# Performance work log

Hardware: AMD Instinct MI355X
Metric: run time of the kernel (lower is better)

The kernel has to match this reference:

```python
import jax, jax.numpy as jnp
import numpy as np

B, C, H, W = 8, 512, 64, 64
HEADS = 8
R = 4  # reduction_ratio: depthwise conv kernel=stride=R, padding=R//2
EPS = 1e-5


def _conv(x, w, stride=1, pad=0, groups=1):
    # NCHW / OIHW conv
    return jax.lax.conv_general_dilated(
        x, w, (stride, stride), ((pad, pad), (pad, pad)),
        feature_group_count=groups)


def _layernorm_ch(x, g, b):
    # channel-wise LayerNorm over dim=1 (biased variance, as torch.var(unbiased=False))
    mean = jnp.mean(x, axis=1, keepdims=True)
    var = jnp.var(x, axis=1, keepdims=True)
    return (x - mean) / jnp.sqrt(var + EPS) * g + b


def _to_kv(t, wkv_dw, ln_g, ln_b, wkv_pw):
    t = _conv(t, wkv_dw, stride=R, pad=R // 2, groups=C)  # depthwise strided conv
    t = _layernorm_ch(t, ln_g, ln_b)
    return _conv(t, wkv_pw)  # 1x1 pointwise


def _split_heads(t):
    # 'b (h c) x y -> (b h) (x y) c'
    b, c, x, y = t.shape
    d = c // HEADS
    return t.reshape(b, HEADS, d, x * y).transpose(0, 1, 3, 2).reshape(b * HEADS, x * y, d)


def setup_inputs() -> dict:
    key = jax.random.key(0)
    ks = jax.random.split(key, 7)
    sem = jax.random.normal(ks[0], (B, C, H, W), jnp.float32)
    spa = jax.random.normal(ks[1], (B, C, H, W), jnp.float32)
    x = jax.random.normal(ks[2], (B, C, H, W), jnp.float32)
    wq = jax.random.normal(ks[3], (C, C, 1, 1), jnp.float32) * 0.02
    wkv_dw = jax.random.normal(ks[4], (C, 1, R, R), jnp.float32) * 0.02  # depthwise, groups=C
    ln_g = jnp.ones((1, C, 1, 1), jnp.float32)
    ln_b = jnp.zeros((1, C, 1, 1), jnp.float32)
    wkv_pw = jax.random.normal(ks[5], (C, C, 1, 1), jnp.float32) * 0.02
    wout = jax.random.normal(ks[6], (C, C, 1, 1), jnp.float32) * 0.02
    return {"sem": sem, "spa": spa, "x": x, "wq": wq, "wkv_dw": wkv_dw,
            "ln_g": ln_g, "ln_b": ln_b, "wkv_pw": wkv_pw, "wout": wout}


def reference(sem, spa, x, wq, wkv_dw, ln_g, ln_b, wkv_pw, wout):
    h, w = x.shape[-2:]
    scale = (C // HEADS) ** -0.5
    q = _conv(sem, wq)                               # [B,C,H,W]
    k = _to_kv(spa, wkv_dw, ln_g, ln_b, wkv_pw)      # [B,C,H',W'] downsampled
    v = _to_kv(x, wkv_dw, ln_g, ln_b, wkv_pw)
    q, k, v = map(_split_heads, (q, k, v))           # [(B*h), N, d]
    dots = jnp.einsum('bid,bjd->bij', q, k) * scale  # [(B*h), Nq, Nk]
    attn = jax.nn.softmax(dots, axis=-1)
    out = jnp.einsum('bij,bjd->bid', attn, v)        # [(B*h), Nq, d]
    # '(b h) (x y) c -> b (h c) x y'
    d = C // HEADS
    out = out.reshape(B, HEADS, h * w, d).transpose(0, 1, 3, 2).reshape(B, C, h, w)
    return _conv(out, wout)
```

## Files before the change

kernel.cpp:

```cpp
#include <hip/hip_runtime.h>
#include <hip/hip_bf16.h>


#define BATCH 8
#define CH 512
#define HW 4096
#define NHEADS 8
#define HD 64
#define PP 289
#define NKP 320

typedef __attribute__((ext_vector_type(8))) short bf16x8;
typedef __attribute__((ext_vector_type(4))) float f32x4;

__device__ inline float sanitize(float x) {
    unsigned u = __float_as_uint(x);
    if ((u & 0x7F800000u) == 0x7F800000u) return 0.0f;
    return x;
}
__device__ inline float ldin(const void* p, size_t i, int f32) {
    float x = f32 ? ((const float*)p)[i]
                  : __bfloat162float(((const __hip_bfloat16*)p)[i]);
    return sanitize(x);
}
__device__ inline void stout(void* p, size_t i, float v, int f32) {
    if (f32) ((float*)p)[i] = v;
    else     ((__hip_bfloat16*)p)[i] = __float2bfloat16(v);
}
__device__ inline short f2bf(float x) {
    unsigned u = __float_as_uint(x);
    unsigned r = (u + 0x7FFFu + ((u >> 16) & 1u)) >> 16;
    return (short)r;
}
__device__ inline float bf2f(short s) {
    unsigned u = ((unsigned)(unsigned short)s) << 16;
    return __uint_as_float(u);
}
__device__ inline void gload_lds16(const void* g, void* l) {
    __builtin_amdgcn_global_load_lds(
        (const __attribute__((address_space(1))) void*)g,
        (__attribute__((address_space(3))) void*)l, 16, 0, 0);
}

__global__ void detect_dtype(const unsigned short* __restrict__ w, int* __restrict__ flag) {
    __shared__ int red[256];
    int tid = threadIdx.x;
    int cnt = 0;
    for (int i = tid; i < 8192; i += 256) {
        unsigned e = w[i] & 0x7F80u;
        cnt += (e >= 0x4300u) ? 1 : 0;
    }
    red[tid] = cnt;
    __syncthreads();
    for (int o = 128; o; o >>= 1) { if (tid < o) red[tid] += red[tid + o]; __syncthreads(); }
    if (tid == 0) *flag = (red[0] > 500) ? 1 : 0;
}

__global__ __launch_bounds__(256)
void cvt_w(const void* __restrict__ in, short* __restrict__ out, const int* __restrict__ flag) {
    const int f32 = *flag;
    int i = (blockIdx.x * 256 + threadIdx.x) * 8;
#pragma unroll
    for (int e = 0; e < 8; ++e) out[i + e] = f2bf(ldin(in, i + e, f32));
}

__global__ __launch_bounds__(256)
void wprep(const void* __restrict__ w, const void* __restrict__ g, const void* __restrict__ bb,
           short* __restrict__ wg, float* __restrict__ ws, float* __restrict__ wb,
           const int* __restrict__ flag) {
    const int f32 = *flag;
    const int tid = threadIdx.x;
    const int wave = tid >> 6, lane = tid & 63;
    const int m = blockIdx.x * 4 + wave;
    float s = 0.f, sb = 0.f;
    union { alignas(16) short sh[8]; int4 v; } u;
#pragma unroll
    for (int e = 0; e < 8; ++e) {
        int c = lane * 8 + e;
        float wv = ldin(w, (size_t)m * CH + c, f32);
        float gv = ldin(g, c, f32);
        float bv = ldin(bb, c, f32);
        float p = wv * gv;
        u.sh[e] = f2bf(p);
        s += p;
        sb += wv * bv;
    }
    *(int4*)(wg + (size_t)m * CH + lane * 8) = u.v;
#pragma unroll
    for (int o = 1; o < 64; o <<= 1) {
        s += __shfl_xor(s, o, 64);
        sb += __shfl_xor(sb, o, 64);
    }
    if (lane == 0) { ws[m] = s; wb[m] = sb; }
}

__global__ __launch_bounds__(256)
void transpose_cvt(const void* __restrict__ in, short* __restrict__ outT,
                   const int* __restrict__ flag) {
    __shared__ short T[64 * 72];
    const int f32 = *flag;
    const int tid = threadIdx.x;
    const int z = blockIdx.z;
    const int c0 = blockIdx.y * 64, p0 = blockIdx.x * 64;
    {
        int c = tid >> 2, ps = (tid & 3) * 16;
        size_t src = ((size_t)z * CH + c0 + c) * HW + p0 + ps;
        short* dst = &T[c * 72 + ps];
        if (f32) {
            const float4* fp = (const float4*)((const float*)in + src);
#pragma unroll
            for (int v = 0; v < 4; ++v) {
                float4 w4 = fp[v];
                dst[v * 4 + 0] = f2bf(sanitize(w4.x));
                dst[v * 4 + 1] = f2bf(sanitize(w4.y));
                dst[v * 4 + 2] = f2bf(sanitize(w4.z));
                dst[v * 4 + 3] = f2bf(sanitize(w4.w));
            }
        } else {
            const int4* ip = (const int4*)((const short*)in + src);
#pragma unroll
            for (int v = 0; v < 2; ++v) {
                union { int4 q; short s[8]; } u; u.q = ip[v];
#pragma unroll
                for (int e = 0; e < 8; ++e) {
                    short sv = u.s[e];
                    if ((sv & 0x7F80) == 0x7F80) sv = 0;
                    dst[v * 8 + e] = sv;
                }
            }
        }
    }
    __syncthreads();
    {
        int p = tid >> 2, cs = (tid & 3) * 16;
        union { short s[16]; int4 v[2]; } u;
#pragma unroll
        for (int e = 0; e < 16; ++e) u.s[e] = T[(cs + e) * 72 + p];
        short* op = outT + ((size_t)z * HW + p0 + p) * CH + c0 + cs;
        *(int4*)op = u.v[0];
        *(int4*)(op + 8) = u.v[1];
    }
}

__global__ __launch_bounds__(256)
void dwconv(const void* __restrict__ in, const void* __restrict__ w,
            float* __restrict__ out, const int* __restrict__ flag) {
    __shared__ float T[4096];
    __shared__ float wf[16];
    const int f32 = *flag;
    const int tid = threadIdx.x;
    const int bc = blockIdx.x;
    const int c = bc & (CH - 1);
    size_t ibase = (size_t)bc * HW;
    if (tid < 16) wf[tid] = ldin(w, (size_t)c * 16 + tid, f32);
    if (f32) {
        const float4* ip = (const float4*)((const float*)in + ibase);
#pragma unroll
        for (int k = 0; k < 4; ++k) {
            float4 v = ip[k * 256 + tid];
            float* d = &T[(k * 256 + tid) * 4];
            d[0] = sanitize(v.x); d[1] = sanitize(v.y);
            d[2] = sanitize(v.z); d[3] = sanitize(v.w);
        }
    } else {
        const int4* ip = (const int4*)((const short*)in + ibase);
#pragma unroll
        for (int k = 0; k < 2; ++k) {
            union { int4 q; unsigned short s[8]; } u; u.q = ip[k * 256 + tid];
            float* d = &T[(k * 256 + tid) * 8];
#pragma unroll
            for (int e = 0; e < 8; ++e) {
                unsigned short sv = u.s[e];
                if ((sv & 0x7F80u) == 0x7F80u) sv = 0;
                d[e] = __bfloat162float(*(__hip_bfloat16*)&sv);
            }
        }
    }
    __syncthreads();
    for (int o = tid; o < PP; o += 256) {
        int oy = o / 17, ox = o % 17;
        float s = 0.f;
#pragma unroll
        for (int ky = 0; ky < 4; ++ky) {
            int iy = oy * 4 - 2 + ky;
            if ((unsigned)iy >= 64u) continue;
#pragma unroll
            for (int kx = 0; kx < 4; ++kx) {
                int ix = ox * 4 - 2 + kx;
                if ((unsigned)ix >= 64u) continue;
                s += T[iy * 64 + ix] * wf[ky * 4 + kx];
            }
        }
        out[(size_t)bc * PP + o] = s;
    }
}

__global__ __launch_bounds__(256)
void transpose_kv(const float* __restrict__ tk, const float* __restrict__ tv,
                  short* __restrict__ tT) {
    __shared__ short T[64 * 72];
    const int tid = threadIdx.x;
    const int zz = blockIdx.z;
    const float* src = (zz < 8 ? tk : tv) + (size_t)(zz & 7) * CH * PP;
    const int c0 = blockIdx.y * 64, p0 = blockIdx.x * 64;
    {
        int c = tid >> 2, ps = (tid & 3) * 16;
        const float* sp = src + (size_t)(c0 + c) * PP + p0 + ps;
        short* dst = &T[c * 72 + ps];
#pragma unroll
        for (int e = 0; e < 16; ++e) {
            int pos = p0 + ps + e;
            dst[e] = (pos < PP) ? f2bf(sp[e]) : (short)0;
        }
    }
    __syncthreads();
    {
        int p = tid >> 2, cs = (tid & 3) * 16;
        union { short s[16]; int4 v[2]; } u;
#pragma unroll
        for (int e = 0; e < 16; ++e) u.s[e] = T[(cs + e) * 72 + p];
        short* op = tT + ((size_t)zz * NKP + p0 + p) * CH + c0 + cs;
        *(int4*)op = u.v[0];
        *(int4*)(op + 8) = u.v[1];
    }
}

__global__ __launch_bounds__(256)
void kv_stats(const short* __restrict__ tT, float* __restrict__ mean,
              float* __restrict__ rstd) {
    const int tid = threadIdx.x;
    const int wave = tid >> 6, lane = tid & 63;
    const int zz = blockIdx.y;
    const int pos = blockIdx.x * 4 + wave;
    bf16x8 v = *(const bf16x8*)(tT + ((size_t)zz * NKP + pos) * CH + lane * 8);
    float s = 0.f, sq = 0.f;
#pragma unroll
    for (int e = 0; e < 8; ++e) {
        float x = bf2f(v[e]);
        s += x; sq += x * x;
    }
#pragma unroll
    for (int o = 1; o < 64; o <<= 1) {
        s += __shfl_xor(s, o, 64);
        sq += __shfl_xor(sq, o, 64);
    }
    if (lane == 0) {
        float m = s * (1.0f / 512.0f);
        float var = sq * (1.0f / 512.0f) - m * m;
        mean[zz * NKP + pos] = m;
        rstd[zz * NKP + pos] = rsqrtf(fmaxf(var, 0.f) + 1e-5f);
    }
}

__global__ __launch_bounds__(256)
void kv_mfma(const short* __restrict__ wg, const short* __restrict__ tT,
             const float* __restrict__ mean, const float* __restrict__ rstd,
             const float* __restrict__ ws, const float* __restrict__ wb,
             short* __restrict__ kpack, short* __restrict__ vpack) {
    __shared__ short Alds[64 * 32];
    __shared__ short Blds[64 * 32];
    const int tid = threadIdx.x;
    const int wave = tid >> 6, lane = tid & 63;
    const int quad = lane >> 4, l15 = lane & 15;
    const int n0 = blockIdx.x * 64, m0 = blockIdx.y * 64;
    const int zz = blockIdx.z;
    const int row = tid >> 2, koff = (tid & 3) * 8;

    f32x4 acc[4];
#pragma unroll
    for (int nf = 0; nf < 4; ++nf) acc[nf] = (f32x4){0.f, 0.f, 0.f, 0.f};

    const short* abase = wg + (size_t)(m0 + row) * CH + koff;
    const short* bbase = tT + ((size_t)zz * NKP + n0 + row) * CH + koff;
    short* al = Alds + row * 32 + koff;
    short* bl = Blds + row * 32 + koff;

    for (int k0 = 0; k0 < CH; k0 += 32) {
        gload_lds16(abase + k0, al);
        gload_lds16(bbase + k0, bl);
        __syncthreads();
        bf16x8 af = *(const bf16x8*)(Alds + (wave * 16 + l15) * 32 + quad * 8);
#pragma unroll
        for (int nf = 0; nf < 4; ++nf) {
            bf16x8 bfr = *(const bf16x8*)(Blds + (nf * 16 + l15) * 32 + quad * 8);
            acc[nf] = __builtin_amdgcn_mfma_f32_16x16x32_bf16(af, bfr, acc[nf], 0, 0, 0);
        }
        __syncthreads();
    }
    const int b = zz & 7;
    const bool isv = zz >= 8;
    float wsv[4], wbv[4];
#pragma unroll
    for (int i = 0; i < 4; ++i) {
        int m = m0 + wave * 16 + quad * 4 + i;
        wsv[i] = ws[m];
        wbv[i] = wb[m];
    }
#pragma unroll
    for (int nf = 0; nf < 4; ++nf) {
        int n = n0 + nf * 16 + l15;
        float mu = mean[zz * NKP + n];
        float rs = rstd[zz * NKP + n];
        bool vld = n < PP;
#pragma unroll
        for (int i = 0; i < 4; ++i) {
            int m = m0 + wave * 16 + quad * 4 + i;
            int head = m >> 6, d = m & 63;
            int bh = b * NHEADS + head;
            float val = vld ? (rs * (acc[nf][i] - mu * wsv[i]) + wbv[i]) : 0.f;
            short sv = f2bf(val);
            if (!isv) kpack[(((size_t)bh * 8 + (d >> 3)) * NKP + n) * 8 + (d & 7)] = sv;
            else      vpack[(((size_t)bh * 40 + (n >> 3)) * HD + d) * 8 + (n & 7)] = sv;
        }
    }
}

__global__ __launch_bounds__(256)
void gemm_mfma(const short* __restrict__ A, const short* __restrict__ Bt,
               void* __restrict__ Cout, const int* __restrict__ flag, int epi) {
    __shared__ short Alds[128 * 32];
    __shared__ short Blds[128 * 32];
    const int f32 = *flag;
    const int tid = threadIdx.x;
    const int wave = tid >> 6, lane = tid & 63;
    const int quad = lane >> 4, l15 = lane & 15;
    const int wm = wave >> 1, wn = wave & 1;
    const int n0 = blockIdx.x * 128, m0 = blockIdx.y * 128;
    const int z = blockIdx.z;
    const int r4 = tid >> 2;
    const int s8 = (tid & 3) * 8;

    f32x4 acc[4][4];
#pragma unroll
    for (int a = 0; a < 4; ++a)
#pragma unroll
        for (int b = 0; b < 4; ++b) acc[a][b] = (f32x4){0.f, 0.f, 0.f, 0.f};

    const short* abase = A + (size_t)(m0 + r4) * 512 + s8;
    const short* bbase = Bt + ((size_t)z * HW + n0 + r4) * 512 + s8;
    short* al = Alds + r4 * 32 + s8;
    short* bl = Blds + r4 * 32 + s8;

    for (int k0 = 0; k0 < 512; k0 += 32) {
#pragma unroll
        for (int c = 0; c < 2; ++c) {
            gload_lds16(abase + (size_t)(c * 64) * 512 + k0, al + c * 2048);
            gload_lds16(bbase + (size_t)(c * 64) * 512 + k0, bl + c * 2048);
        }
        __syncthreads();
        bf16x8 af[4], bfr[4];
#pragma unroll
        for (int a = 0; a < 4; ++a)
            af[a] = *(const bf16x8*)(Alds + (wm * 64 + a * 16 + l15) * 32 + quad * 8);
#pragma unroll
        for (int b = 0; b < 4; ++b)
            bfr[b] = *(const bf16x8*)(Blds + (wn * 64 + b * 16 + l15) * 32 + quad * 8);
#pragma unroll
        for (int a = 0; a < 4; ++a)
#pragma unroll
            for (int b = 0; b < 4; ++b)
                acc[a][b] = __builtin_amdgcn_mfma_f32_16x16x32_bf16(af[a], bfr[b], acc[a][b], 0, 0, 0);
        __syncthreads();
    }
#pragma unroll
    for (int a = 0; a < 4; ++a) {
        int mb = m0 + wm * 64 + a * 16 + quad * 4;
#pragma unroll
        for (int b = 0; b < 4; ++b) {
            int n = n0 + wn * 64 + b * 16 + l15;
            if (epi == 0) {
#pragma unroll
                for (int i = 0; i < 4; ++i)
                    stout(Cout, ((size_t)z * CH + mb + i) * HW + n, acc[a][b][i], f32);
            } else {
                union { alignas(8) short s[4]; int2 v; } u;
#pragma unroll
                for (int i = 0; i < 4; ++i) u.s[i] = f2bf(acc[a][b][i] * 0.125f);
                int h = mb >> 6, d = mb & 63;
                *(int2*)((short*)Cout + ((size_t)(z * NHEADS + h) * HW + n) * HD + d) = u.v;
            }
        }
    }
}

__global__ __launch_bounds__(512, 2)
void attn_mfma(const short* __restrict__ qt, const short* __restrict__ kpack,
               const short* __restrict__ vpack, short* __restrict__ attT) {
    __shared__ short Klds[8 * NKP * 8];
    __shared__ short Vlds[40 * HD * 8];
    __shared__ short PO[256 * 72];
    const int tid = threadIdx.x;
    const int wave = tid >> 6, lane = tid & 63;
    const int quad = lane >> 4, l15 = lane & 15;
    const int bh = blockIdx.y;

    {
        const short* kbase = kpack + (size_t)bh * 8 * NKP * 8;
        const short* vbase = vpack + (size_t)bh * 40 * HD * 8;
#pragma unroll
        for (int rnd = 0; rnd < 5; ++rnd) {
            int off = (rnd * 512 + tid) * 8;
            gload_lds16(kbase + off, Klds + off);
            gload_lds16(vbase + off, Vlds + off);
        }
    }
    __syncthreads();

    short* pw = PO + (wave * 2) * 640;

    for (int it = 0; it < 2; ++it) {
        const int q0 = blockIdx.x * 512 + it * 256;
        bf16x8 qf[2][2];
#pragma unroll
        for (int r = 0; r < 2; ++r) {
            const short* qp = qt + ((size_t)bh * HW + q0 + wave * 32 + r * 16 + l15) * HD + quad * 8;
            qf[r][0] = *(const bf16x8*)qp;
            qf[r][1] = *(const bf16x8*)(qp + 32);
        }
        f32x4 O[2][4];
        float lsum[2][4];
#pragma unroll
        for (int r = 0; r < 2; ++r)
#pragma unroll
            for (int df = 0; df < 4; ++df) {
                O[r][df] = (f32x4){0.f, 0.f, 0.f, 0.f};
                lsum[r][df] = 0.f;
            }

#pragma unroll
        for (int sc = 0; sc < 10; ++sc) {
            bf16x8 kf0[2], kf1[2], vf[4];
#pragma unroll
            for (int c2 = 0; c2 < 2; ++c2) {
                const short* kp = Klds + ((size_t)quad * NKP + sc * 32 + c2 * 16 + l15) * 8;
                kf0[c2] = *(const bf16x8*)kp;
                kf1[c2] = *(const bf16x8*)(Klds + ((size_t)(4 + quad) * NKP + sc * 32 + c2 * 16 + l15) * 8);
            }
#pragma unroll
            for (int df = 0; df < 4; ++df)
                vf[df] = *(const bf16x8*)(Vlds + (((size_t)(sc * 4 + quad)) * HD + df * 16 + l15) * 8);
#pragma unroll
            for (int r = 0; r < 2; ++r) {
                short* pwr = pw + r * 640;
#pragma unroll
                for (int c2 = 0; c2 < 2; ++c2) {
                    f32x4 zz = (f32x4){0.f, 0.f, 0.f, 0.f};
                    zz = __builtin_amdgcn_mfma_f32_16x16x32_bf16(qf[r][0], kf0[c2], zz, 0, 0, 0);
                    f32x4 sfv = __builtin_amdgcn_mfma_f32_16x16x32_bf16(qf[r][1], kf1[c2], zz, 0, 0, 0);
                    int nk = sc * 32 + c2 * 16 + l15;
                    bool valid = nk < PP;
#pragma unroll
                    for (int i = 0; i < 4; ++i) {
                        float pv = valid ? __expf(fminf(sfv[i], 30.f)) : 0.f;
                        lsum[r][i] += pv;
                        pwr[(quad * 4 + i) * 40 + c2 * 16 + l15] = f2bf(pv);
                    }
                }
            }
            asm volatile("s_waitcnt lgkmcnt(0)" ::: "memory");
            __builtin_amdgcn_sched_barrier(0);
#pragma unroll
            for (int r = 0; r < 2; ++r) {
                bf16x8 pf = *(const bf16x8*)(pw + r * 640 + l15 * 40 + quad * 8);
#pragma unroll
                for (int df = 0; df < 4; ++df)
                    O[r][df] = __builtin_amdgcn_mfma_f32_16x16x32_bf16(pf, vf[df], O[r][df], 0, 0, 0);
            }
            asm volatile("" ::: "memory");
        }
#pragma unroll
        for (int r = 0; r < 2; ++r)
#pragma unroll
            for (int i = 0; i < 4; ++i) {
                float s = lsum[r][i];
                s += __shfl_xor(s, 1, 64);
                s += __shfl_xor(s, 2, 64);
                s += __shfl_xor(s, 4, 64);
                s += __shfl_xor(s, 8, 64);
                lsum[r][i] = 1.0f / s;
            }
        __syncthreads();
#pragma unroll
        for (int r = 0; r < 2; ++r)
#pragma unroll
            for (int df = 0; df < 4; ++df)
#pragma unroll
                for (int i = 0; i < 4; ++i)
                    PO[(wave * 32 + r * 16 + quad * 4 + i) * 72 + df * 16 + l15] =
                        f2bf(O[r][df][i] * lsum[r][i]);
        __syncthreads();
        {
            int q = tid >> 1, half = tid & 1;
            const short* src = PO + q * 72 + half * 32;
            int4 a0 = *(const int4*)(src);
            int4 a1 = *(const int4*)(src + 8);
            int4 a2 = *(const int4*)(src + 16);
            int4 a3 = *(const int4*)(src + 24);
            int b = bh >> 3, h = bh & 7;
            short* op = attT + ((size_t)b * HW + q0 + q) * CH + h * HD + half * 32;
            *(int4*)op = a0;
            *(int4*)(op + 8) = a1;
            *(int4*)(op + 16) = a2;
            *(int4*)(op + 24) = a3;
        }
        __syncthreads();
    }
}

extern "C" void kernel_launch(void* const* d_in, const int* in_sizes, int n_in,
                              void* d_out, int out_size, void* d_ws, size_t ws_size,
                              hipStream_t stream) {
    const void* sem    = d_in[0];
    const void* spa    = d_in[1];
    const void* x      = d_in[2];
    const void* wq     = d_in[3];
    const void* wkv_dw = d_in[4];
    const void* ln_g   = d_in[5];
    const void* ln_b   = d_in[6];
    const void* wkv_pw = d_in[7];
    const void* wout   = d_in[8];

    const size_t nkv = (size_t)BATCH * CH * PP;
    char* p = (char*)d_ws;
    auto alloc = [&](size_t bytes) { char* r = p; p += (bytes + 255) & ~(size_t)255; return r; };
    int*   flag  = (int*)alloc(256);
    float* tk    = (float*)alloc(nkv * 4);
    float* tv    = (float*)alloc(nkv * 4);
    short* kpk   = (short*)alloc((size_t)64 * 8 * NKP * 8 * 2);
    short* vpk   = (short*)alloc((size_t)64 * 40 * HD * 8 * 2);
    short* semT  = (short*)alloc((size_t)BATCH * HW * CH * 2);
    short* attT  = (short*)alloc((size_t)BATCH * HW * CH * 2);
    short* wqb   = (short*)alloc((size_t)512 * 512 * 2);
    short* woutb = (short*)alloc((size_t)512 * 512 * 2);
    short* qt    = (short*)d_out;

    short* tT    = (short*)d_out;
    short* wg    = attT;
    float* ws    = (float*)(attT + (size_t)512 * 512);
    float* wb    = ws + 512;
    float* meanp = wb + 512;
    float* rstdp = meanp + 16 * NKP;

    detect_dtype<<<1, 256, 0, stream>>>((const unsigned short*)sem, flag);

    cvt_w<<<128, 256, 0, stream>>>(wq, wqb, flag);
    cvt_w<<<128, 256, 0, stream>>>(wout, woutb, flag);
    wprep<<<128, 256, 0, stream>>>(wkv_pw, ln_g, ln_b, wg, ws, wb, flag);

    dim3 gt(HW / 64, CH / 64, BATCH);
    transpose_cvt<<<gt, 256, 0, stream>>>(sem, semT, flag);

    dwconv<<<BATCH * CH, 256, 0, stream>>>(spa, wkv_dw, tk, flag);
    dwconv<<<BATCH * CH, 256, 0, stream>>>(x,   wkv_dw, tv, flag);

    dim3 gtk(NKP / 64, CH / 64, 16);
    transpose_kv<<<gtk, 256, 0, stream>>>(tk, tv, tT);

    dim3 gs(NKP / 4, 16);
    kv_stats<<<gs, 256, 0, stream>>>(tT, meanp, rstdp);

    dim3 gkv(NKP / 64, CH / 64, 16);
    kv_mfma<<<gkv, 256, 0, stream>>>(wg, tT, meanp, rstdp, ws, wb, kpk, vpk);

    dim3 gg(HW / 128, CH / 128, BATCH);
    gemm_mfma<<<gg, 256, 0, stream>>>(wqb, semT, qt, flag, 1);

    dim3 ga(HW / 512, 64);
    attn_mfma<<<ga, 512, 0, stream>>>(qt, kpk, vpk, attT);

    gemm_mfma<<<gg, 256, 0, stream>>>(woutb, attT, d_out, flag, 0);
}
```

Before: 403.1 us.

## Enlarge attention blocks, fold log2e into Q scale, swizzle transpose LDS

Measured after the change: 395.7 us. No clear change (-1.8%).

```diff
diff --git a/kernel.cpp b/kernel.cpp
--- a/kernel.cpp
+++ b/kernel.cpp
@@ -105,37 +105,45 @@
     {
         int c = tid >> 2, ps = (tid & 3) * 16;
         size_t src = ((size_t)z * CH + c0 + c) * HW + p0 + ps;
-        short* dst = &T[c * 72 + ps];
+        union { alignas(16) short s[16]; int4 v[2]; } u;
         if (f32) {
             const float4* fp = (const float4*)((const float*)in + src);
 #pragma unroll
-            for (int v = 0; v < 4; ++v) {
-                float4 w4 = fp[v];
-                dst[v * 4 + 0] = f2bf(sanitize(w4.x));
-                dst[v * 4 + 1] = f2bf(sanitize(w4.y));
-                dst[v * 4 + 2] = f2bf(sanitize(w4.z));
-                dst[v * 4 + 3] = f2bf(sanitize(w4.w));
+            for (int v4 = 0; v4 < 4; ++v4) {
+                float4 w4 = fp[v4];
+                u.s[v4 * 4 + 0] = f2bf(sanitize(w4.x));
+                u.s[v4 * 4 + 1] = f2bf(sanitize(w4.y));
+                u.s[v4 * 4 + 2] = f2bf(sanitize(w4.z));
+                u.s[v4 * 4 + 3] = f2bf(sanitize(w4.w));
             }
         } else {
             const int4* ip = (const int4*)((const short*)in + src);
 #pragma unroll
-            for (int v = 0; v < 2; ++v) {
-                union { int4 q; short s[8]; } u; u.q = ip[v];
+            for (int v4 = 0; v4 < 2; ++v4) {
+                union { int4 q; short s[8]; } t; t.q = ip[v4];
 #pragma unroll
                 for (int e = 0; e < 8; ++e) {
-                    short sv = u.s[e];
+                    short sv = t.s[e];
                     if ((sv & 0x7F80) == 0x7F80) sv = 0;
-                    dst[v * 8 + e] = sv;
+                    u.s[v4 * 8 + e] = sv;
                 }
             }
         }
+        int base = c * 144 + ps * 2;
+        int k = ((c >> 4) & 3) << 4;
+        *(int4*)((char*)T + (base ^ k)) = u.v[0];
+        *(int4*)((char*)T + ((base + 16) ^ k)) = u.v[1];
     }
     __syncthreads();
     {
         int p = tid >> 2, cs = (tid & 3) * 16;
         union { short s[16]; int4 v[2]; } u;
 #pragma unroll
-        for (int e = 0; e < 16; ++e) u.s[e] = T[(cs + e) * 72 + p];
+        for (int e = 0; e < 16; ++e) {
+            int row = cs + e;
+            int byte = row * 144 + p * 2;
+            u.s[e] = *(const short*)((const char*)T + (byte ^ (((row >> 4) & 3) << 4)));
+        }
         short* op = outT + ((size_t)z * HW + p0 + p) * CH + c0 + cs;
         *(int4*)op = u.v[0];
         *(int4*)(op + 8) = u.v[1];
@@ -375,7 +383,7 @@
             } else {
                 union { alignas(8) short s[4]; int2 v; } u;
 #pragma unroll
-                for (int i = 0; i < 4; ++i) u.s[i] = f2bf(acc[a][b][i] * 0.125f);
+                for (int i = 0; i < 4; ++i) u.s[i] = f2bf(acc[a][b][i] * 0.18033688011f);
                 int h = mb >> 6, d = mb & 63;
                 *(int2*)((short*)Cout + ((size_t)(z * NHEADS + h) * HW + n) * HD + d) = u.v;
             }
@@ -383,33 +391,32 @@
     }
 }
 
-__global__ __launch_bounds__(512, 2)
+__global__ __launch_bounds__(1024, 1)
 void attn_mfma(const short* __restrict__ qt, const short* __restrict__ kpack,
                const short* __restrict__ vpack, short* __restrict__ attT) {
     __shared__ short Klds[8 * NKP * 8];
     __shared__ short Vlds[40 * HD * 8];
-    __shared__ short PO[256 * 72];
+    __shared__ short PO[20480];
     const int tid = threadIdx.x;
     const int wave = tid >> 6, lane = tid & 63;
     const int quad = lane >> 4, l15 = lane & 15;
     const int bh = blockIdx.y;
+    const int b = bh >> 3, h = bh & 7;
 
     {
-        const short* kbase = kpack + (size_t)bh * 8 * NKP * 8;
-        const short* vbase = vpack + (size_t)bh * 40 * HD * 8;
-#pragma unroll
-        for (int rnd = 0; rnd < 5; ++rnd) {
-            int off = (rnd * 512 + tid) * 8;
-            gload_lds16(kbase + off, Klds + off);
-            gload_lds16(vbase + off, Vlds + off);
+        const short* kbase = kpack + (size_t)bh * (8 * NKP * 8);
+        const short* vbase = vpack + (size_t)bh * (40 * HD * 8);
+        for (int i = tid; i < 2560; i += 1024) {
+            gload_lds16(kbase + i * 8, Klds + i * 8);
+            gload_lds16(vbase + i * 8, Vlds + i * 8);
         }
     }
     __syncthreads();
 
-    short* pw = PO + (wave * 2) * 640;
+    short* pw = PO + wave * 1280;
 
     for (int it = 0; it < 2; ++it) {
-        const int q0 = blockIdx.x * 512 + it * 256;
+        const int q0 = blockIdx.x * 1024 + it * 512;
         bf16x8 qf[2][2];
 #pragma unroll
         for (int r = 0; r < 2; ++r) {
@@ -447,11 +454,9 @@
                     f32x4 zz = (f32x4){0.f, 0.f, 0.f, 0.f};
                     zz = __builtin_amdgcn_mfma_f32_16x16x32_bf16(qf[r][0], kf0[c2], zz, 0, 0, 0);
                     f32x4 sfv = __builtin_amdgcn_mfma_f32_16x16x32_bf16(qf[r][1], kf1[c2], zz, 0, 0, 0);
-                    int nk = sc * 32 + c2 * 16 + l15;
-                    bool valid = nk < PP;
 #pragma unroll
                     for (int i = 0; i < 4; ++i) {
-                        float pv = valid ? __expf(fminf(sfv[i], 30.f)) : 0.f;
+                        float pv = __builtin_amdgcn_exp2f(fminf(sfv[i], 43.f));
                         lsum[r][i] += pv;
                         pwr[(quad * 4 + i) * 40 + c2 * 16 + l15] = f2bf(pv);
                     }
@@ -459,6 +464,7 @@
             }
             asm volatile("s_waitcnt lgkmcnt(0)" ::: "memory");
             __builtin_amdgcn_sched_barrier(0);
+            __builtin_amdgcn_s_setprio(1);
 #pragma unroll
             for (int r = 0; r < 2; ++r) {
                 bf16x8 pf = *(const bf16x8*)(pw + r * 640 + l15 * 40 + quad * 8);
@@ -466,6 +472,7 @@
                 for (int df = 0; df < 4; ++df)
                     O[r][df] = __builtin_amdgcn_mfma_f32_16x16x32_bf16(pf, vf[df], O[r][df], 0, 0, 0);
             }
+            __builtin_amdgcn_s_setprio(0);
             asm volatile("" ::: "memory");
         }
 #pragma unroll
@@ -477,33 +484,34 @@
                 s += __shfl_xor(s, 2, 64);
                 s += __shfl_xor(s, 4, 64);
                 s += __shfl_xor(s, 8, 64);
-                lsum[r][i] = 1.0f / s;
+                lsum[r][i] = 1.0f / (s - 31.0f);
             }
         __syncthreads();
 #pragma unroll
-        for (int r = 0; r < 2; ++r)
-#pragma unroll
-            for (int df = 0; df < 4; ++df)
-#pragma unroll
-                for (int i = 0; i < 4; ++i)
-                    PO[(wave * 32 + r * 16 + quad * 4 + i) * 72 + df * 16 + l15] =
-                        f2bf(O[r][df][i] * lsum[r][i]);
-        __syncthreads();
-        {
-            int q = tid >> 1, half = tid & 1;
-            const short* src = PO + q * 72 + half * 32;
-            int4 a0 = *(const int4*)(src);
-            int4 a1 = *(const int4*)(src + 8);
-            int4 a2 = *(const int4*)(src + 16);
-            int4 a3 = *(const int4*)(src + 24);
-            int b = bh >> 3, h = bh & 7;
-            short* op = attT + ((size_t)b * HW + q0 + q) * CH + h * HD + half * 32;
-            *(int4*)op = a0;
-            *(int4*)(op + 8) = a1;
-            *(int4*)(op + 16) = a2;
-            *(int4*)(op + 24) = a3;
-        }
-        __syncthreads();
+        for (int hp = 0; hp < 2; ++hp) {
+            if ((wave >> 3) == hp) {
+                int wl = wave & 7;
+#pragma unroll
+                for (int r = 0; r < 2; ++r)
+#pragma unroll
+                    for (int df = 0; df < 4; ++df)
+#pragma unroll
+                        for (int i = 0; i < 4; ++i)
+                            PO[(wl * 32 + r * 16 + quad * 4 + i) * 72 + df * 16 + l15] =
+                                f2bf(O[r][df][i] * lsum[r][i]);
+            }
+            __syncthreads();
+            {
+                int q = tid >> 2, seg = tid & 3;
+                const short* src = PO + q * 72 + seg * 16;
+                int4 a0 = *(const int4*)(src);
+                int4 a1 = *(const int4*)(src + 8);
+                short* op = attT + ((size_t)b * HW + q0 + hp * 256 + q) * CH + h * HD + seg * 16;
+                *(int4*)op = a0;
+                *(int4*)(op + 8) = a1;
+            }
+            __syncthreads();
+        }
     }
 }
 
@@ -565,8 +573,8 @@
     dim3 gg(HW / 128, CH / 128, BATCH);
     gemm_mfma<<<gg, 256, 0, stream>>>(wqb, semT, qt, flag, 1);
 
-    dim3 ga(HW / 512, 64);
-    attn_mfma<<<ga, 512, 0, stream>>>(qt, kpk, vpk, attT);
+    dim3 ga(HW / 1024, 64);
+    attn_mfma<<<ga, 1024, 0, stream>>>(qt, kpk, vpk, attT);
 
     gemm_mfma<<<gg, 256, 0, stream>>>(woutb, attT, d_out, flag, 0);
 }
```
